# Kernel optimization log

Measured on AMD Instinct MI355X. Metric: run time of the kernel, lower is better.

The kernel has to match this reference:

```python
import jax, jax.numpy as jnp
import numpy as np

H = 1024
T = 4096
B = 16

def setup_inputs() -> dict:
    key = jax.random.key(0)
    k1, k2, k3 = jax.random.split(key, 3)
    dec_hidden = jax.random.normal(k1, (H, B), dtype=jnp.float32)
    encoder_outputs = jax.random.normal(k2, (T, B, H), dtype=jnp.float32)
    # nn.Linear(H, H, bias=False) weight, torch default init: U(-1/sqrt(H), 1/sqrt(H)), shape [out, in]
    bound = 1.0 / np.sqrt(H)
    W = jax.random.uniform(k3, (H, H), minval=-bound, maxval=bound, dtype=jnp.float32)
    return {"dec_hidden": dec_hidden, "encoder_outputs": encoder_outputs, "W": W}

def reference(dec_hidden, encoder_outputs, W):
    # method == 'general': score[b, t] = dec_hidden[:, b] . (W @ encoder_outputs[t, b])
    # Linear: y = x @ W.T, W is [out, in]
    proj = jnp.einsum('tbh,dh->tbd', encoder_outputs, W)       # [T, B, H]
    scores = jnp.einsum('hb,tbh->bt', dec_hidden, proj)        # [B, T]
    return jax.nn.softmax(scores, axis=1)
```

## Files before the change

kernel.cpp:

```cpp
#include <hip/hip_runtime.h>
#include <math.h>

#define H 1024
#define T 4096
#define B 16

typedef float f4 __attribute__((ext_vector_type(4)));

__global__ void __launch_bounds__(256) proj_vec_kernel(
    const float* __restrict__ dec, const float* __restrict__ W,
    float* __restrict__ v)
{
    int b     = blockIdx.x >> 4;
    int htile = blockIdx.x & 15;
    int h4    = threadIdx.x & 15;
    int dc    = threadIdx.x >> 4;
    int h4base = htile * 16;

    const f4* Wp = (const f4*)W;
    f4 acc = {0.f, 0.f, 0.f, 0.f};
    int d0 = dc * 64;
    #pragma unroll 8
    for (int i = 0; i < 64; ++i) {
        int d = d0 + i;
        float s = dec[d * B + b];
        f4 w = Wp[d * (H / 4) + h4base + h4];
        acc += s * w;
    }

    __shared__ f4 red[256];
    red[threadIdx.x] = acc;
    __syncthreads();
    #pragma unroll
    for (int s = 8; s > 0; s >>= 1) {
        if (dc < s) {
            f4 m = red[dc * 16 + h4] + red[(dc + s) * 16 + h4];
            red[dc * 16 + h4] = m;
        }
        __syncthreads();
    }
    if (dc == 0) {
        ((f4*)(v + b * H))[h4base + h4] = red[h4];
    }
}

__global__ void __launch_bounds__(256) scores_kernel(
    const float* __restrict__ v, const float* __restrict__ enc,
    float* __restrict__ scores)
{
    int wave = (int)((blockIdx.x * 256u + threadIdx.x) >> 6);
    int lane = threadIdx.x & 63;
    int b = wave & (B - 1);
    int t = wave >> 4;
    const f4* ep = (const f4*)(enc + (size_t)t * (B * H) + (size_t)b * H);
    const f4* vp = (const f4*)(v + b * H);
    float acc = 0.f;
    #pragma unroll
    for (int i = 0; i < 4; ++i) {
        f4 e = __builtin_nontemporal_load(&ep[lane + i * 64]);
        f4 w = vp[lane + i * 64];
        acc = fmaf(e.x, w.x, acc);
        acc = fmaf(e.y, w.y, acc);
        acc = fmaf(e.z, w.z, acc);
        acc = fmaf(e.w, w.w, acc);
    }
    #pragma unroll
    for (int off = 32; off > 0; off >>= 1)
        acc += __shfl_down(acc, off);
    if (lane == 0) scores[b * T + t] = acc;
}

__global__ void __launch_bounds__(256) softmax_kernel(
    const float* __restrict__ scores, float* __restrict__ out)
{
    int b = blockIdx.x;
    int tid = threadIdx.x;
    __shared__ float red[8];
    const f4* rp = (const f4*)(scores + (size_t)b * T);
    f4 vals[4];
    float m = -INFINITY;
    #pragma unroll
    for (int i = 0; i < 4; ++i) {
        vals[i] = rp[tid + i * 256];
        m = fmaxf(m, fmaxf(fmaxf(vals[i].x, vals[i].y), fmaxf(vals[i].z, vals[i].w)));
    }
    #pragma unroll
    for (int off = 32; off > 0; off >>= 1)
        m = fmaxf(m, __shfl_down(m, off));
    if ((tid & 63) == 0) red[tid >> 6] = m;
    __syncthreads();
    m = fmaxf(fmaxf(red[0], red[1]), fmaxf(red[2], red[3]));

    float s = 0.f;
    #pragma unroll
    for (int i = 0; i < 4; ++i) {
        vals[i].x = __expf(vals[i].x - m);
        vals[i].y = __expf(vals[i].y - m);
        vals[i].z = __expf(vals[i].z - m);
        vals[i].w = __expf(vals[i].w - m);
        s += vals[i].x + vals[i].y + vals[i].z + vals[i].w;
    }
    #pragma unroll
    for (int off = 32; off > 0; off >>= 1)
        s += __shfl_down(s, off);
    if ((tid & 63) == 0) red[4 + (tid >> 6)] = s;
    __syncthreads();
    float inv = 1.f / (red[4] + red[5] + red[6] + red[7]);

    f4* op = (f4*)(out + (size_t)b * T);
    #pragma unroll
    for (int i = 0; i < 4; ++i) {
        f4 r = vals[i] * inv;
        op[tid + i * 256] = r;
    }
}

extern "C" void kernel_launch(void* const* d_in, const int* in_sizes, int n_in,
                              void* d_out, int out_size, void* d_ws, size_t ws_size,
                              hipStream_t stream)
{
    const float* dec = (const float*)d_in[0];
    const float* enc = (const float*)d_in[1];
    const float* W   = (const float*)d_in[2];
    float* out = (float*)d_out;

    float* v      = (float*)d_ws;
    float* scores = v + B * H;

    proj_vec_kernel<<<256, 256, 0, stream>>>(dec, W, v);
    scores_kernel<<<(T * B) / 4, 256, 0, stream>>>(v, enc, scores);
    softmax_kernel<<<B, 256, 0, stream>>>(scores, out);
}
```

Before: 53.07 us.

## Fuse softmax into scores kernel via last-block atomic counter; retile projection kernel

```diff
diff --git a/kernel.cpp b/kernel.cpp
--- a/kernel.cpp
+++ b/kernel.cpp
@@ -7,21 +7,24 @@
 
 typedef float f4 __attribute__((ext_vector_type(4)));
 
+
 __global__ void __launch_bounds__(256) proj_vec_kernel(
     const float* __restrict__ dec, const float* __restrict__ W,
-    float* __restrict__ v)
+    float* __restrict__ v, int* __restrict__ cnt)
 {
-    int b     = blockIdx.x >> 4;
-    int htile = blockIdx.x & 15;
-    int h4    = threadIdx.x & 15;
-    int dc    = threadIdx.x >> 4;
-    int h4base = htile * 16;
+    if (blockIdx.x == 0 && threadIdx.x < B) cnt[threadIdx.x * 32] = 0;
+
+    int b      = blockIdx.x >> 5;
+    int htile  = blockIdx.x & 31;
+    int h4     = threadIdx.x & 7;
+    int dc     = threadIdx.x >> 3;
+    int h4base = htile * 8;
 
     const f4* Wp = (const f4*)W;
     f4 acc = {0.f, 0.f, 0.f, 0.f};
-    int d0 = dc * 64;
+    int d0 = dc * 32;
     #pragma unroll 8
-    for (int i = 0; i < 64; ++i) {
+    for (int i = 0; i < 32; ++i) {
         int d = d0 + i;
         float s = dec[d * B + b];
         f4 w = Wp[d * (H / 4) + h4base + h4];
@@ -32,26 +35,26 @@
     red[threadIdx.x] = acc;
     __syncthreads();
     #pragma unroll
-    for (int s = 8; s > 0; s >>= 1) {
+    for (int s = 16; s > 0; s >>= 1) {
         if (dc < s) {
-            f4 m = red[dc * 16 + h4] + red[(dc + s) * 16 + h4];
-            red[dc * 16 + h4] = m;
+            f4 m = red[dc * 8 + h4] + red[(dc + s) * 8 + h4];
+            red[dc * 8 + h4] = m;
         }
         __syncthreads();
     }
-    if (dc == 0) {
+    if (dc == 0)
         ((f4*)(v + b * H))[h4base + h4] = red[h4];
-    }
 }
 
-__global__ void __launch_bounds__(256) scores_kernel(
+__global__ void __launch_bounds__(256) scores_softmax_kernel(
     const float* __restrict__ v, const float* __restrict__ enc,
-    float* __restrict__ scores)
+    float* scores, int* cnt, float* out)
 {
     int wave = (int)((blockIdx.x * 256u + threadIdx.x) >> 6);
     int lane = threadIdx.x & 63;
     int b = wave & (B - 1);
     int t = wave >> 4;
+
     const f4* ep = (const f4*)(enc + (size_t)t * (B * H) + (size_t)b * H);
     const f4* vp = (const f4*)(v + b * H);
     float acc = 0.f;
@@ -67,51 +70,62 @@
     #pragma unroll
     for (int off = 32; off > 0; off >>= 1)
         acc += __shfl_down(acc, off);
-    if (lane == 0) scores[b * T + t] = acc;
-}
 
-__global__ void __launch_bounds__(256) softmax_kernel(
-    const float* __restrict__ scores, float* __restrict__ out)
-{
-    int b = blockIdx.x;
-    int tid = threadIdx.x;
-    __shared__ float red[8];
-    const f4* rp = (const f4*)(scores + (size_t)b * T);
-    f4 vals[4];
-    float m = -INFINITY;
-    #pragma unroll
-    for (int i = 0; i < 4; ++i) {
-        vals[i] = rp[tid + i * 256];
-        m = fmaxf(m, fmaxf(fmaxf(vals[i].x, vals[i].y), fmaxf(vals[i].z, vals[i].w)));
-    }
-    #pragma unroll
-    for (int off = 32; off > 0; off >>= 1)
-        m = fmaxf(m, __shfl_down(m, off));
-    if ((tid & 63) == 0) red[tid >> 6] = m;
+    if (lane == 0)
+        __hip_atomic_store(&scores[(size_t)b * T + t], acc,
+                           __ATOMIC_RELAXED, __HIP_MEMORY_SCOPE_AGENT);
+
     __syncthreads();
-    m = fmaxf(fmaxf(red[0], red[1]), fmaxf(red[2], red[3]));
 
-    float s = 0.f;
-    #pragma unroll
-    for (int i = 0; i < 4; ++i) {
-        vals[i].x = __expf(vals[i].x - m);
-        vals[i].y = __expf(vals[i].y - m);
-        vals[i].z = __expf(vals[i].z - m);
-        vals[i].w = __expf(vals[i].w - m);
-        s += vals[i].x + vals[i].y + vals[i].z + vals[i].w;
-    }
-    #pragma unroll
-    for (int off = 32; off > 0; off >>= 1)
-        s += __shfl_down(s, off);
-    if ((tid & 63) == 0) red[4 + (tid >> 6)] = s;
-    __syncthreads();
-    float inv = 1.f / (red[4] + red[5] + red[6] + red[7]);
+    if (threadIdx.x < 64) {
+        int last = 0;
+        if (lane < 4) {
+            int bb = (blockIdx.x * 4 + lane) & (B - 1);
+            int old = atomicAdd(&cnt[bb * 32], 1);
+            last = (old == T - 1);
+        }
+        unsigned long long mask = __ballot(last);
+        while (mask) {
+            int p = __ffsll(mask) - 1;
+            mask &= mask - 1;
+            int bb = (blockIdx.x * 4 + p) & (B - 1);
 
-    f4* op = (f4*)(out + (size_t)b * T);
-    #pragma unroll
-    for (int i = 0; i < 4; ++i) {
-        f4 r = vals[i] * inv;
-        op[tid + i * 256] = r;
+            const f4* rp = (const f4*)(scores + (size_t)bb * T);
+            float m = -INFINITY, s = 0.f;
+            #pragma unroll 4
+            for (int i = 0; i < 16; ++i) {
+                f4 x = rp[lane + i * 64];
+                float xm = fmaxf(fmaxf(x.x, x.y), fmaxf(x.z, x.w));
+                float mn = fmaxf(m, xm);
+                s = s * __expf(m - mn)
+                    + __expf(x.x - mn) + __expf(x.y - mn)
+                    + __expf(x.z - mn) + __expf(x.w - mn);
+                m = mn;
+            }
+            #pragma unroll
+            for (int off = 32; off > 0; off >>= 1) {
+                float mo = __shfl_xor(m, off);
+                float so = __shfl_xor(s, off);
+                float mn = fmaxf(m, mo);
+                s = s * __expf(m - mn) + so * __expf(mo - mn);
+                m = mn;
+            }
+            float inv = 1.f / s;
+
+            asm volatile("" ::: "memory");
+
+            f4* op = (f4*)(out + (size_t)bb * T);
+            #pragma unroll 4
+            for (int i = 0; i < 16; ++i) {
+                f4 x = rp[lane + i * 64];
+                f4 r;
+                r.x = __expf(x.x - m) * inv;
+                r.y = __expf(x.y - m) * inv;
+                r.z = __expf(x.z - m) * inv;
+                r.w = __expf(x.w - m) * inv;
+                op[lane + i * 64] = r;
+            }
+        }
     }
 }
 
@@ -126,8 +140,8 @@
 
     float* v      = (float*)d_ws;
     float* scores = v + B * H;
+    int*   cnt    = (int*)(scores + B * T);
 
-    proj_vec_kernel<<<256, 256, 0, stream>>>(dec, W, v);
-    scores_kernel<<<(T * B) / 4, 256, 0, stream>>>(v, enc, scores);
-    softmax_kernel<<<B, 256, 0, stream>>>(scores, out);
+    proj_vec_kernel<<<512, 256, 0, stream>>>(dec, W, v, cnt);
+    scores_softmax_kernel<<<(T * B) / 4, 256, 0, stream>>>(v, enc, scores, cnt, out);
 }
```

Measured after the change: 93.50 us. +76.2%, slower.
